# Kernel optimization log

Measured on AMD Instinct MI355X. Metric: run time of the kernel, lower is better.

## Reference

```python
import jax, jax.numpy as jnp
import numpy as np

D_HIDDEN = 1024
D_MODEL = 1024
R_MIN, R_MAX = 0.0, 1.0
MAX_PHASE = 6.28
SEQ_LEN = 16384


def setup_inputs() -> dict:
    key = jax.random.key(0)
    k_in, k_th, k_nu, k_bre, k_bim, k_cre, k_cim, k_d = jax.random.split(key, 8)
    inputs = jax.random.normal(k_in, (SEQ_LEN, D_MODEL), dtype=jnp.float32)
    # theta_log ~ log(max_phase * U)
    u_th = jax.random.uniform(k_th, (D_HIDDEN,), dtype=jnp.float32)
    theta_log = jnp.log(MAX_PHASE * u_th)
    # nu_log ~ log(-0.5 * log(U*(r_max^2 - r_min^2) + r_min^2))
    u_nu = jax.random.uniform(k_nu, (D_HIDDEN,), dtype=jnp.float32)
    nu_log = jnp.log(-0.5 * jnp.log(u_nu * (R_MAX**2 - R_MIN**2) + R_MIN**2))
    # gamma_log = log(sqrt(1 - |lambda|^2))
    diag_lambda = jnp.exp(-jnp.exp(nu_log) + 1j * jnp.exp(theta_log))
    gamma_log = jnp.log(jnp.sqrt(1.0 - jnp.abs(diag_lambda) ** 2))
    norm_b = jnp.sqrt(2.0 * D_MODEL)
    norm_c = jnp.sqrt(1.0 * D_HIDDEN)
    B_re = jax.random.normal(k_bre, (D_HIDDEN, D_MODEL), dtype=jnp.float32) / norm_b
    B_im = jax.random.normal(k_bim, (D_HIDDEN, D_MODEL), dtype=jnp.float32) / norm_b
    C_re = jax.random.normal(k_cre, (D_MODEL, D_HIDDEN), dtype=jnp.float32) / norm_c
    C_im = jax.random.normal(k_cim, (D_MODEL, D_HIDDEN), dtype=jnp.float32) / norm_c
    Dp = jax.random.normal(k_d, (D_MODEL,), dtype=jnp.float32)
    return {"inputs": inputs, "nu_log": nu_log, "theta_log": theta_log,
            "gamma_log": gamma_log, "B_re": B_re, "B_im": B_im,
            "C_re": C_re, "C_im": C_im, "Dp": Dp}


def _binop(q_i, q_j):
    # elementwise associative op for diagonal linear recurrence
    A_i, b_i = q_i
    A_j, b_j = q_j
    return (A_j * A_i, A_j * b_i + b_j)


def reference(inputs, nu_log, theta_log, gamma_log, B_re, B_im, C_re, C_im, Dp):
    # diag_lambda: [H] complex64
    diag_lambda = jnp.exp(-jnp.exp(nu_log) + 1j * jnp.exp(theta_log))
    B_norm = (B_re + 1j * B_im) * jnp.exp(gamma_log)[:, None]  # [H, D]
    C = C_re + 1j * C_im                                        # [D, H]
    L = inputs.shape[0]
    # Bu_t = B_norm @ x_t  -> [L, H] complex
    Bu = inputs.astype(B_norm.dtype) @ B_norm.T
    Lambda = jnp.broadcast_to(diag_lambda[None, :], (L, diag_lambda.shape[0]))
    # parallel scan of h_t = lambda * h_{t-1} + Bu_t (initial state = 0)
    _, hidden = jax.lax.associative_scan(_binop, (Lambda, Bu))  # [L, H]
    # y_t = Re[C h_t] + D * x_t
    outputs = jnp.real(hidden @ C.T) + Dp * inputs              # [L, D]
    return (hidden[-1:], outputs)
```

## Files before the change

kernel.cpp:

```cpp
#include <hip/hip_runtime.h>
#include <stdint.h>
#include <stddef.h>

typedef _Float16 f16;
typedef __attribute__((ext_vector_type(8))) _Float16 f16x8;
typedef __attribute__((ext_vector_type(4))) _Float16 f16x4;
typedef __attribute__((ext_vector_type(4))) float f32x4;
typedef __attribute__((ext_vector_type(2))) float f32x2;

#define L_SEQ 16384
#define DH    1024
#define DM    1024
#define NH2   2048
#define NC    256
#define LC    (L_SEQ / NC)

#define WSCALE     64.0f
#define INV_WSCALE 0.015625f

__device__ __forceinline__ void async_copy16(const void* g, void* l) {
  __builtin_amdgcn_global_load_lds((const __attribute__((address_space(1))) void*)g,
                                   (__attribute__((address_space(3))) void*)l,
                                   16, 0, 0);
}

__device__ __forceinline__ float h_lo(uint32_t w) {
  uint16_t u = (uint16_t)(w & 0xffffu); f16 h; __builtin_memcpy(&h, &u, 2); return (float)h;
}
__device__ __forceinline__ float h_hi(uint32_t w) {
  uint16_t u = (uint16_t)(w >> 16); f16 h; __builtin_memcpy(&h, &u, 2); return (float)h;
}

#define NB_CAST 8192
#define NB_W    1024
__global__ void k_prep_all(const float* __restrict__ x, f16* __restrict__ xb,
                           const float* __restrict__ B_re, const float* __restrict__ B_im,
                           const float* __restrict__ gamma_log, f16* __restrict__ Wcat,
                           const float* __restrict__ C_re, const float* __restrict__ C_im,
                           f16* __restrict__ Ccat,
                           const float* __restrict__ nu_log,
                           const float* __restrict__ theta_log,
                           float* __restrict__ lam_re, float* __restrict__ lam_im,
                           float* __restrict__ lamC_re, float* __restrict__ lamC_im) {
  const int b = blockIdx.x;
  if (b < NB_CAST) {
    int i = (b * 256 + (int)threadIdx.x) * 8;
    const float4 a0 = *(const float4*)(x + i);
    const float4 a1 = *(const float4*)(x + i + 4);
    f16x8 v;
    v[0] = (f16)a0.x; v[1] = (f16)a0.y; v[2] = (f16)a0.z; v[3] = (f16)a0.w;
    v[4] = (f16)a1.x; v[5] = (f16)a1.y; v[6] = (f16)a1.z; v[7] = (f16)a1.w;
    *(f16x8*)(xb + i) = v;
  } else if (b < NB_CAST + NB_W) {
    int idx = ((b - NB_CAST) * 256 + (int)threadIdx.x) * 4;
    int h = idx / DM;
    int d = idx - h * DM;
    float g = expf(gamma_log[h]) * WSCALE;
    float4 re = *(const float4*)(B_re + idx);
    float4 im = *(const float4*)(B_im + idx);
    f16x4 vr, vi;
    vr[0] = (f16)(re.x * g); vr[1] = (f16)(re.y * g);
    vr[2] = (f16)(re.z * g); vr[3] = (f16)(re.w * g);
    vi[0] = (f16)(im.x * g); vi[1] = (f16)(im.y * g);
    vi[2] = (f16)(im.z * g); vi[3] = (f16)(im.w * g);
    *(f16x4*)(Wcat + (size_t)(2 * h) * DM + d)     = vr;
    *(f16x4*)(Wcat + (size_t)(2 * h + 1) * DM + d) = vi;
  } else if (b < NB_CAST + 2 * NB_W) {
    int idx = ((b - NB_CAST - NB_W) * 256 + (int)threadIdx.x) * 4;
    int d = idx / DH;
    int k = idx - d * DH;
    float4 re = *(const float4*)(C_re + idx);
    float4 im = *(const float4*)(C_im + idx);
    f16x8 v;
    v[0] = (f16)re.x; v[1] = (f16)(-im.x);
    v[2] = (f16)re.y; v[3] = (f16)(-im.y);
    v[4] = (f16)re.z; v[5] = (f16)(-im.z);
    v[6] = (f16)re.w; v[7] = (f16)(-im.w);
    *(f16x8*)(Ccat + (size_t)d * NH2 + 2 * k) = v;
  } else {
    int h = (b - NB_CAST - 2 * NB_W) * 256 + (int)threadIdx.x;
    if (h < DH) {
      float nu  = expf(nu_log[h]);
      float th  = expf(theta_log[h]);
      float mag = expf(-nu);
      float lr = mag * cosf(th);
      float li = mag * sinf(th);
      lam_re[h] = lr; lam_im[h] = li;
      float ar = lr, ai = li;
#pragma unroll
      for (int i = 0; i < 6; ++i) {
        float nr = ar * ar - ai * ai;
        float ni = 2.f * ar * ai;
        ar = nr; ai = ni;
      }
      lamC_re[h] = ar; lamC_im[h] = ai;
    }
  }
}

template <int MODE>
__global__ __launch_bounds__(256, 3)
void k_gemm(const f16* __restrict__ A, const f16* __restrict__ B,
            void* __restrict__ Cout, const float* __restrict__ x,
            const float* __restrict__ dp,
            const float* __restrict__ lam_re, const float* __restrict__ lam_im,
            float* __restrict__ chunk_end, int K, int N) {
  __shared__ char smem[32768];
  f16* As = (f16*)smem;
  f16* Bs = (f16*)(smem + 16384);
  const int tid  = threadIdx.x;
  const int lane = tid & 63;
  const int wave = tid >> 6;
  const int wm = wave >> 1, wn = wave & 1;
  const int quad = lane >> 4;
  const int l16  = lane & 15;

  const int lin = blockIdx.y * gridDim.x + blockIdx.x;
  const int nY  = gridDim.y;
  const int per = 8 * nY;
  const int sg  = lin / per;
  const int r   = lin - sg * per;
  const int bx  = sg * 8 + (r & 7);
  const int by  = r >> 3;
  const int m0 = bx * 128;
  const int n0 = by * 128;

  f32x4 acc[4][4];
#pragma unroll
  for (int i = 0; i < 4; ++i)
#pragma unroll
    for (int j = 0; j < 4; ++j)
      acc[i][j] = f32x4{0.f, 0.f, 0.f, 0.f};

  for (int k0 = 0; k0 < K; k0 += 64) {
    __syncthreads();
#pragma unroll
    for (int q = 0; q < 4; ++q) {
      const int c = q * 256 + tid;
      const int row = c >> 3, slot = c & 7;
      const int part = slot ^ (row & 7);
      async_copy16(A + (size_t)(m0 + row) * K + k0 + part * 8, (char*)As + c * 16);
      async_copy16(B + (size_t)(n0 + row) * K + k0 + part * 8, (char*)Bs + c * 16);
    }
    __syncthreads();
#pragma unroll
    for (int kk = 0; kk < 64; kk += 32) {
      const int pbase = (kk >> 3);
      f16x8 fa[4], fb[4];
#pragma unroll
      for (int i = 0; i < 4; ++i) {
        const int ra = wm * 64 + i * 16 + l16;
        const int rb = wn * 64 + i * 16 + l16;
        const int sa = (pbase + quad) ^ (ra & 7);
        const int sb = (pbase + quad) ^ (rb & 7);
        fa[i] = *(const f16x8*)(As + ra * 64 + sa * 8);
        fb[i] = *(const f16x8*)(Bs + rb * 64 + sb * 8);
      }
#pragma unroll
      for (int i = 0; i < 4; ++i)
#pragma unroll
        for (int j = 0; j < 4; ++j)
          acc[i][j] = __builtin_amdgcn_mfma_f32_16x16x32_f16(fa[i], fb[j], acc[i][j], 0, 0, 0);
    }
  }

  if (MODE == 0) {
    __syncthreads();
    f16* T = (f16*)smem;
#pragma unroll
    for (int i = 0; i < 4; ++i)
#pragma unroll
      for (int j = 0; j < 4; ++j) {
        const int col = wn * 64 + j * 16 + l16;
        const int grp = col >> 3, cin = col & 7;
#pragma unroll
        for (int p = 0; p < 4; ++p) {
          const int row = wm * 64 + i * 16 + quad * 4 + p;
          T[row * 128 + ((grp ^ (row & 7)) << 3) + cin] = (f16)acc[i][j][p];
        }
      }
    __syncthreads();
    f16* out = (f16*)Cout;
    {
      const int row = tid >> 1, half = tid & 1;
#pragma unroll
      for (int o = 0; o < 8; ++o) {
        const int grp = half * 8 + o;
        f16x8 v = *(const f16x8*)(T + row * 128 + ((grp ^ (row & 7)) << 3));
        *(f16x8*)(out + (size_t)(m0 + row) * N + n0 + grp * 8) = v;
      }
    }
    if (tid < 128) {
      const int ck = tid >> 6;
      const int ch = tid & 63;
      const int gch = (n0 >> 1) + ch;
      const float lr = lam_re[gch], li = lam_im[gch];
      float hr = 0.f, hi = 0.f;
#pragma unroll 8
      for (int t = 0; t < 64; ++t) {
        const int row = ck * 64 + t;
        const int grpsw = ((ch >> 2) ^ (row & 7)) << 3;
        uint32_t w = *(const uint32_t*)(T + row * 128 + grpsw + ((2 * ch) & 7));
        float br = h_lo(w), bi = h_hi(w);
        float nr = lr * hr - li * hi + br;
        float ni = lr * hi + li * hr + bi;
        hr = nr; hi = ni;
      }
      *(f32x2*)(chunk_end + (size_t)(2 * bx + ck) * NH2 + n0 + 2 * ch) = f32x2{hr, hi};
    }
  } else {
    float* out = (float*)Cout;
    const int crow0 = m0 + wm * 64 + quad * 4;
    const int ccol0 = n0 + wn * 64 + l16;
#pragma unroll
    for (int j = 0; j < 4; ++j) {
      const int col = ccol0 + j * 16;
      const float dpv = dp[col];
#pragma unroll
      for (int i = 0; i < 4; ++i)
#pragma unroll
        for (int p = 0; p < 4; ++p) {
          const int row = crow0 + i * 16 + p;
          out[(size_t)row * N + col] = acc[i][j][p] + dpv * x[(size_t)row * N + col];
        }
    }
  }
}

__global__ void k_scan_carry(const float* __restrict__ chunk_end,
                             const float* __restrict__ lamC_re,
                             const float* __restrict__ lamC_im,
                             float* __restrict__ carry_in,
                             float* __restrict__ out_final,
                             int interleave) {
  const int h = blockIdx.x * 256 + threadIdx.x;
  const float lr = lamC_re[h], li = lamC_im[h];
  float er = 0.f, ei = 0.f;
#pragma unroll 16
  for (int c = 0; c < NC; ++c) {
    *(f32x2*)(carry_in + (size_t)c * NH2 + 2 * h) = f32x2{er, ei};
    f32x2 ce = *(const f32x2*)(chunk_end + (size_t)c * NH2 + 2 * h);
    float nr = lr * er - li * ei + ce[0];
    float ni = lr * ei + li * er + ce[1];
    er = nr; ei = ni;
  }
  if (interleave) {
    *(f32x2*)(out_final + 2 * h) = f32x2{er * INV_WSCALE, ei * INV_WSCALE};
  } else {
    out_final[h] = er * INV_WSCALE;
  }
}

__global__ void k_scan_apply(f16* __restrict__ Bu,
                             const float* __restrict__ lam_re,
                             const float* __restrict__ lam_im,
                             const float* __restrict__ carry_in) {
  const int colbase = (blockIdx.y * 256 + (int)threadIdx.x) * 4;
  const int c = blockIdx.x;
  const int h0 = colbase >> 1;
  const float lr0 = lam_re[h0],     li0 = lam_im[h0];
  const float lr1 = lam_re[h0 + 1], li1 = lam_im[h0 + 1];
  f32x4 cv = *(const f32x4*)(carry_in + (size_t)c * NH2 + colbase);
  float hr0 = cv[0], hi0 = cv[1], hr1 = cv[2], hi1 = cv[3];
  f16* p = Bu + (size_t)c * LC * NH2 + colbase;
#pragma unroll 4
  for (int t = 0; t < LC; ++t) {
    f16x4 b = *(const f16x4*)(p);
    float nr0 = lr0 * hr0 - li0 * hi0 + (float)b[0];
    float ni0 = lr0 * hi0 + li0 * hr0 + (float)b[1];
    float nr1 = lr1 * hr1 - li1 * hi1 + (float)b[2];
    float ni1 = lr1 * hi1 + li1 * hr1 + (float)b[3];
    hr0 = nr0; hi0 = ni0; hr1 = nr1; hi1 = ni1;
    f16x4 wv;
    wv[0] = (f16)(hr0 * INV_WSCALE); wv[1] = (f16)(hi0 * INV_WSCALE);
    wv[2] = (f16)(hr1 * INV_WSCALE); wv[3] = (f16)(hi1 * INV_WSCALE);
    *(f16x4*)(p) = wv;
    p += NH2;
  }
}


extern "C" void kernel_launch(void* const* d_in, const int* in_sizes, int n_in,
                              void* d_out, int out_size, void* d_ws, size_t ws_size,
                              hipStream_t stream) {
  const float* inputs    = (const float*)d_in[0];
  const float* nu_log    = (const float*)d_in[1];
  const float* theta_log = (const float*)d_in[2];
  const float* gamma_log = (const float*)d_in[3];
  const float* B_re      = (const float*)d_in[4];
  const float* B_im      = (const float*)d_in[5];
  const float* C_re      = (const float*)d_in[6];
  const float* C_im      = (const float*)d_in[7];
  const float* Dp        = (const float*)d_in[8];

  char* ws = (char*)d_ws;
  float* lam_re    = (float*)(ws + 0);
  float* lam_im    = (float*)(ws + 4096);
  float* lamC_re   = (float*)(ws + 8192);
  float* lamC_im   = (float*)(ws + 12288);
  float* chunk_end = (float*)(ws + 65536);
  float* carry_in  = (float*)(ws + 65536 + (2u << 20));
  f16*   Wcat      = (f16*)  (ws + 65536 + (4u << 20));
  f16*   Ccat      = (f16*)  (ws + 65536 + (8u << 20));
  f16*   Xb        = (f16*)  (ws + 65536 + (12u << 20));
  f16*   Bu        = (f16*)  (ws + 65536 + (44u << 20));

  int interleave = 1;
  int state_floats = 2048;
  if (out_size == 1024 + L_SEQ * DM) { interleave = 0; state_floats = 1024; }

  float* out_state = (float*)d_out;
  float* out_y     = (float*)d_out + state_floats;

  k_prep_all<<<dim3(NB_CAST + 2 * NB_W + 4), dim3(256), 0, stream>>>(
      inputs, Xb, B_re, B_im, gamma_log, Wcat, C_re, C_im, Ccat,
      nu_log, theta_log, lam_re, lam_im, lamC_re, lamC_im);

  k_gemm<0><<<dim3(L_SEQ / 128, NH2 / 128), dim3(256), 0, stream>>>(
      Xb, Wcat, (void*)Bu, nullptr, nullptr, lam_re, lam_im, chunk_end, DM, NH2);

  k_scan_carry<<<dim3(4), dim3(256), 0, stream>>>(chunk_end, lamC_re, lamC_im,
                                                  carry_in, out_state, interleave);
  k_scan_apply<<<dim3(NC, 2), dim3(256), 0, stream>>>(Bu, lam_re, lam_im, carry_in);

  k_gemm<1><<<dim3(L_SEQ / 128, DM / 128), dim3(256), 0, stream>>>(
      Bu, Ccat, (void*)out_y, inputs, Dp, nullptr, nullptr, nullptr, NH2, DM);

  (void)in_sizes; (void)n_in; (void)ws_size;
}
```

Measured before the change: 388.1 us.

## Use 256x256 GEMM tiles with 8 waves and double-buffered async LDS pipeline

Both GEMM instantiations move from 128x128 tiles with 4 waves to 256x256 tiles with 8 waves and 128KB of shared memory. The new K loop double-buffers LDS and issues global-to-LDS copies in quarter-tile steps interleaved with MFMA phases, coordinated by explicit vmcnt/lgkmcnt waits, barriers and setprio. The aim is to raise data reuse per tile and hide global load latency behind matrix math. In exchange, occupancy drops to one block per CU, and the grid for the second GEMM shrinks to 256 blocks, which can leave tail or load-imbalance effects. The epilogue and the per-chunk scan are rewritten for the larger tile.

```diff
diff --git a/kernel.cpp b/kernel.cpp
--- a/kernel.cpp
+++ b/kernel.cpp
@@ -99,21 +99,21 @@
 }
 
 template <int MODE>
-__global__ __launch_bounds__(256, 3)
+__global__ __launch_bounds__(512, 1)
 void k_gemm(const f16* __restrict__ A, const f16* __restrict__ B,
             void* __restrict__ Cout, const float* __restrict__ x,
             const float* __restrict__ dp,
             const float* __restrict__ lam_re, const float* __restrict__ lam_im,
             float* __restrict__ chunk_end, int K, int N) {
-  __shared__ char smem[32768];
-  f16* As = (f16*)smem;
-  f16* Bs = (f16*)(smem + 16384);
+  __shared__ char smem[131072];
   const int tid  = threadIdx.x;
   const int lane = tid & 63;
   const int wave = tid >> 6;
-  const int wm = wave >> 1, wn = wave & 1;
+  const int wm = wave >> 2;
+  const int wn = wave & 3;
   const int quad = lane >> 4;
   const int l16  = lane & 15;
+  const int k7   = l16 & 7;
 
   const int lin = blockIdx.y * gridDim.x + blockIdx.x;
   const int nY  = gridDim.y;
@@ -122,61 +122,152 @@
   const int r   = lin - sg * per;
   const int bx  = sg * 8 + (r & 7);
   const int by  = r >> 3;
-  const int m0 = bx * 128;
-  const int n0 = by * 128;
-
-  f32x4 acc[4][4];
-#pragma unroll
-  for (int i = 0; i < 4; ++i)
+  const int m0 = bx * 256;
+  const int n0 = by * 256;
+
+  const int NT = K >> 6;
+
+  f32x4 acc[8][4];
+#pragma unroll
+  for (int i = 0; i < 8; ++i)
 #pragma unroll
     for (int j = 0; j < 4; ++j)
       acc[i][j] = f32x4{0.f, 0.f, 0.f, 0.f};
 
-  for (int k0 = 0; k0 < K; k0 += 64) {
-    __syncthreads();
-#pragma unroll
-    for (int q = 0; q < 4; ++q) {
-      const int c = q * 256 + tid;
+  auto stage_half = [&](int H) {
+    if (H >= 4 * NT) return;
+    const int tau  = H >> 2;
+    const int part = H & 3;
+    const int d    = tau & 1;
+    const int kcol = tau << 6;
+    const f16* gsrc; int rbase; char* lbase;
+    if (part < 2) { gsrc = B; rbase = n0 + (part << 7);
+                    lbase = (char*)smem + d * 65536 + 32768 + (part << 14); }
+    else          { gsrc = A; rbase = m0 + ((part - 2) << 7);
+                    lbase = (char*)smem + d * 65536 + ((part - 2) << 14); }
+#pragma unroll
+    for (int q = 0; q < 2; ++q) {
+      const int c = (q << 9) + tid;
       const int row = c >> 3, slot = c & 7;
-      const int part = slot ^ (row & 7);
-      async_copy16(A + (size_t)(m0 + row) * K + k0 + part * 8, (char*)As + c * 16);
-      async_copy16(B + (size_t)(n0 + row) * K + k0 + part * 8, (char*)Bs + c * 16);
-    }
-    __syncthreads();
-#pragma unroll
-    for (int kk = 0; kk < 64; kk += 32) {
-      const int pbase = (kk >> 3);
-      f16x8 fa[4], fb[4];
-#pragma unroll
-      for (int i = 0; i < 4; ++i) {
-        const int ra = wm * 64 + i * 16 + l16;
-        const int rb = wn * 64 + i * 16 + l16;
-        const int sa = (pbase + quad) ^ (ra & 7);
-        const int sb = (pbase + quad) ^ (rb & 7);
-        fa[i] = *(const f16x8*)(As + ra * 64 + sa * 8);
-        fb[i] = *(const f16x8*)(Bs + rb * 64 + sb * 8);
-      }
-#pragma unroll
-      for (int i = 0; i < 4; ++i)
-#pragma unroll
-        for (int j = 0; j < 4; ++j)
-          acc[i][j] = __builtin_amdgcn_mfma_f32_16x16x32_f16(fa[i], fb[j], acc[i][j], 0, 0, 0);
-    }
+      const int p = slot ^ (row & 7);
+      async_copy16(gsrc + (size_t)(rbase + row) * K + kcol + (p << 3), lbase + c * 16);
+    }
+  };
+
+  for (int H = 0; H < 7; ++H) stage_half(H);
+  asm volatile("s_waitcnt vmcnt(6)" ::: "memory");
+  __builtin_amdgcn_s_barrier();
+
+  for (int t = 0; t < NT; ++t) {
+    const f16* Asd = (const f16*)((char*)smem + (t & 1) * 65536);
+    const f16* Bsd = Asd + 16384;
+
+    f16x8 bfr[4][2], afr[4][2];
+
+#pragma unroll
+    for (int nf = 0; nf < 4; ++nf) {
+      const int rb = (wn << 6) + (nf << 4) + l16;
+#pragma unroll
+      for (int kq = 0; kq < 2; ++kq) {
+        const int sb = ((kq << 2) | quad) ^ k7;
+        bfr[nf][kq] = *(const f16x8*)(Bsd + rb * 64 + sb * 8);
+      }
+    }
+#pragma unroll
+    for (int mf = 0; mf < 4; ++mf) {
+      const int ra = (wm << 7) + (mf << 4) + l16;
+#pragma unroll
+      for (int kq = 0; kq < 2; ++kq) {
+        const int sa = ((kq << 2) | quad) ^ k7;
+        afr[mf][kq] = *(const f16x8*)(Asd + ra * 64 + sa * 8);
+      }
+    }
+    stage_half(4 * t + 7);
+    __builtin_amdgcn_s_barrier();
+    asm volatile("s_waitcnt lgkmcnt(0)" ::: "memory");
+    __builtin_amdgcn_sched_barrier(0);
+    __builtin_amdgcn_s_setprio(1);
+#pragma unroll
+    for (int mf = 0; mf < 4; ++mf)
+#pragma unroll
+      for (int nf = 0; nf < 2; ++nf)
+#pragma unroll
+        for (int kq = 0; kq < 2; ++kq)
+          acc[mf][nf] = __builtin_amdgcn_mfma_f32_16x16x32_f16(afr[mf][kq], bfr[nf][kq], acc[mf][nf], 0, 0, 0);
+    __builtin_amdgcn_s_setprio(0);
+    __builtin_amdgcn_sched_barrier(0);
+    __builtin_amdgcn_s_barrier();
+
+    stage_half(4 * t + 8);
+    __builtin_amdgcn_s_barrier();
+    __builtin_amdgcn_s_setprio(1);
+#pragma unroll
+    for (int mf = 0; mf < 4; ++mf)
+#pragma unroll
+      for (int nf = 2; nf < 4; ++nf)
+#pragma unroll
+        for (int kq = 0; kq < 2; ++kq)
+          acc[mf][nf] = __builtin_amdgcn_mfma_f32_16x16x32_f16(afr[mf][kq], bfr[nf][kq], acc[mf][nf], 0, 0, 0);
+    __builtin_amdgcn_s_setprio(0);
+    __builtin_amdgcn_sched_barrier(0);
+    __builtin_amdgcn_s_barrier();
+
+#pragma unroll
+    for (int mf = 0; mf < 4; ++mf) {
+      const int ra = (wm << 7) + 64 + (mf << 4) + l16;
+#pragma unroll
+      for (int kq = 0; kq < 2; ++kq) {
+        const int sa = ((kq << 2) | quad) ^ k7;
+        afr[mf][kq] = *(const f16x8*)(Asd + ra * 64 + sa * 8);
+      }
+    }
+    stage_half(4 * t + 9);
+    __builtin_amdgcn_s_barrier();
+    asm volatile("s_waitcnt lgkmcnt(0)" ::: "memory");
+    __builtin_amdgcn_sched_barrier(0);
+    __builtin_amdgcn_s_setprio(1);
+#pragma unroll
+    for (int mf = 0; mf < 4; ++mf)
+#pragma unroll
+      for (int nf = 0; nf < 2; ++nf)
+#pragma unroll
+        for (int kq = 0; kq < 2; ++kq)
+          acc[4 + mf][nf] = __builtin_amdgcn_mfma_f32_16x16x32_f16(afr[mf][kq], bfr[nf][kq], acc[4 + mf][nf], 0, 0, 0);
+    __builtin_amdgcn_s_setprio(0);
+    __builtin_amdgcn_sched_barrier(0);
+    __builtin_amdgcn_s_barrier();
+
+    stage_half(4 * t + 10);
+    if (t == NT - 2) { asm volatile("s_waitcnt vmcnt(0)" ::: "memory"); }
+    else             { asm volatile("s_waitcnt vmcnt(6)" ::: "memory"); }
+    __builtin_amdgcn_s_barrier();
+    __builtin_amdgcn_s_setprio(1);
+#pragma unroll
+    for (int mf = 0; mf < 4; ++mf)
+#pragma unroll
+      for (int nf = 2; nf < 4; ++nf)
+#pragma unroll
+        for (int kq = 0; kq < 2; ++kq)
+          acc[4 + mf][nf] = __builtin_amdgcn_mfma_f32_16x16x32_f16(afr[mf][kq], bfr[nf][kq], acc[4 + mf][nf], 0, 0, 0);
+    __builtin_amdgcn_s_setprio(0);
+    __builtin_amdgcn_sched_barrier(0);
+    __builtin_amdgcn_s_barrier();
   }
 
   if (MODE == 0) {
+    asm volatile("s_waitcnt vmcnt(0)" ::: "memory");
     __syncthreads();
     f16* T = (f16*)smem;
 #pragma unroll
-    for (int i = 0; i < 4; ++i)
-#pragma unroll
-      for (int j = 0; j < 4; ++j) {
-        const int col = wn * 64 + j * 16 + l16;
+    for (int mf = 0; mf < 8; ++mf)
+#pragma unroll
+      for (int nf = 0; nf < 4; ++nf) {
+        const int col = (wn << 6) + (nf << 4) + l16;
         const int grp = col >> 3, cin = col & 7;
 #pragma unroll
         for (int p = 0; p < 4; ++p) {
-          const int row = wm * 64 + i * 16 + quad * 4 + p;
-          T[row * 128 + ((grp ^ (row & 7)) << 3) + cin] = (f16)acc[i][j][p];
+          const int row = (wm << 7) + (mf << 4) + (quad << 2) + p;
+          T[row * 256 + ((grp ^ (row & 7)) << 3) + cin] = (f16)acc[mf][nf][p];
         }
       }
     __syncthreads();
@@ -184,44 +275,44 @@
     {
       const int row = tid >> 1, half = tid & 1;
 #pragma unroll
-      for (int o = 0; o < 8; ++o) {
-        const int grp = half * 8 + o;
-        f16x8 v = *(const f16x8*)(T + row * 128 + ((grp ^ (row & 7)) << 3));
-        *(f16x8*)(out + (size_t)(m0 + row) * N + n0 + grp * 8) = v;
-      }
-    }
-    if (tid < 128) {
-      const int ck = tid >> 6;
-      const int ch = tid & 63;
+      for (int o = 0; o < 16; ++o) {
+        const int grp = (half << 4) + o;
+        f16x8 v = *(const f16x8*)(T + row * 256 + ((grp ^ (row & 7)) << 3));
+        *(f16x8*)(out + (size_t)(m0 + row) * N + n0 + (grp << 3)) = v;
+      }
+    }
+    {
+      const int ck = tid >> 7;
+      const int ch = tid & 127;
       const int gch = (n0 >> 1) + ch;
       const float lr = lam_re[gch], li = lam_im[gch];
       float hr = 0.f, hi = 0.f;
 #pragma unroll 8
-      for (int t = 0; t < 64; ++t) {
-        const int row = ck * 64 + t;
-        const int grpsw = ((ch >> 2) ^ (row & 7)) << 3;
-        uint32_t w = *(const uint32_t*)(T + row * 128 + grpsw + ((2 * ch) & 7));
+      for (int tt = 0; tt < 64; ++tt) {
+        const int row = (ck << 6) + tt;
+        const int sw = (((ch >> 2) ^ (row & 7)) << 3) + ((2 * ch) & 7);
+        uint32_t w = *(const uint32_t*)(T + row * 256 + sw);
         float br = h_lo(w), bi = h_hi(w);
         float nr = lr * hr - li * hi + br;
         float ni = lr * hi + li * hr + bi;
         hr = nr; hi = ni;
       }
-      *(f32x2*)(chunk_end + (size_t)(2 * bx + ck) * NH2 + n0 + 2 * ch) = f32x2{hr, hi};
+      *(f32x2*)(chunk_end + (size_t)((bx << 2) + ck) * NH2 + n0 + 2 * ch) = f32x2{hr, hi};
     }
   } else {
     float* out = (float*)Cout;
-    const int crow0 = m0 + wm * 64 + quad * 4;
-    const int ccol0 = n0 + wn * 64 + l16;
-#pragma unroll
-    for (int j = 0; j < 4; ++j) {
-      const int col = ccol0 + j * 16;
+    const int crow0 = m0 + (wm << 7) + (quad << 2);
+    const int ccol0 = n0 + (wn << 6) + l16;
+#pragma unroll
+    for (int nf = 0; nf < 4; ++nf) {
+      const int col = ccol0 + (nf << 4);
       const float dpv = dp[col];
 #pragma unroll
-      for (int i = 0; i < 4; ++i)
+      for (int mf = 0; mf < 8; ++mf)
 #pragma unroll
         for (int p = 0; p < 4; ++p) {
-          const int row = crow0 + i * 16 + p;
-          out[(size_t)row * N + col] = acc[i][j][p] + dpv * x[(size_t)row * N + col];
+          const int row = crow0 + (mf << 4) + p;
+          out[(size_t)row * N + col] = acc[mf][nf][p] + dpv * x[(size_t)row * N + col];
         }
     }
   }
@@ -316,14 +407,14 @@
       inputs, Xb, B_re, B_im, gamma_log, Wcat, C_re, C_im, Ccat,
       nu_log, theta_log, lam_re, lam_im, lamC_re, lamC_im);
 
-  k_gemm<0><<<dim3(L_SEQ / 128, NH2 / 128), dim3(256), 0, stream>>>(
+  k_gemm<0><<<dim3(L_SEQ / 256, NH2 / 256), dim3(512), 0, stream>>>(
       Xb, Wcat, (void*)Bu, nullptr, nullptr, lam_re, lam_im, chunk_end, DM, NH2);
 
   k_scan_carry<<<dim3(4), dim3(256), 0, stream>>>(chunk_end, lamC_re, lamC_im,
                                                   carry_in, out_state, interleave);
   k_scan_apply<<<dim3(NC, 2), dim3(256), 0, stream>>>(Bu, lam_re, lam_im, carry_in);
 
-  k_gemm<1><<<dim3(L_SEQ / 128, DM / 128), dim3(256), 0, stream>>>(
+  k_gemm<1><<<dim3(L_SEQ / 256, DM / 256), dim3(512), 0, stream>>>(
       Bu, Ccat, (void*)out_y, inputs, Dp, nullptr, nullptr, nullptr, NH2, DM);
 
   (void)in_sizes; (void)n_in; (void)ws_size;
```

After: 426.2 us. 1.1x slower.

## Parallelize chunk-carry scan with Hillis-Steele and read fp16 input in output epilogue

Applied to the files above, without the earlier changes.

The carry scan across chunks used to run on only 4 blocks, with each thread walking 256 chunks one after another. It now launches one block per hidden channel, with one thread per chunk, and runs a log-step Hillis-Steele scan in shared memory using powers of lambda^64. The output GEMM epilogue now reads the fp16 copy of the inputs instead of fp32 for the D*x skip term, which halves that read traffic. The fp16 skip term loses precision, and the log-depth scan changes the floating-point summation order.

```diff
diff --git a/kernel.cpp b/kernel.cpp
--- a/kernel.cpp
+++ b/kernel.cpp
@@ -101,7 +101,7 @@
 template <int MODE>
 __global__ __launch_bounds__(256, 3)
 void k_gemm(const f16* __restrict__ A, const f16* __restrict__ B,
-            void* __restrict__ Cout, const float* __restrict__ x,
+            void* __restrict__ Cout, const void* __restrict__ x,
             const float* __restrict__ dp,
             const float* __restrict__ lam_re, const float* __restrict__ lam_im,
             float* __restrict__ chunk_end, int K, int N) {
@@ -210,6 +210,7 @@
     }
   } else {
     float* out = (float*)Cout;
+    const f16* xb = (const f16*)x;
     const int crow0 = m0 + wm * 64 + quad * 4;
     const int ccol0 = n0 + wn * 64 + l16;
 #pragma unroll
@@ -221,7 +222,7 @@
 #pragma unroll
         for (int p = 0; p < 4; ++p) {
           const int row = crow0 + i * 16 + p;
-          out[(size_t)row * N + col] = acc[i][j][p] + dpv * x[(size_t)row * N + col];
+          out[(size_t)row * N + col] = acc[i][j][p] + dpv * (float)xb[(size_t)row * N + col];
         }
     }
   }
@@ -233,21 +234,37 @@
                              float* __restrict__ carry_in,
                              float* __restrict__ out_final,
                              int interleave) {
-  const int h = blockIdx.x * 256 + threadIdx.x;
-  const float lr = lamC_re[h], li = lamC_im[h];
-  float er = 0.f, ei = 0.f;
-#pragma unroll 16
-  for (int c = 0; c < NC; ++c) {
-    *(f32x2*)(carry_in + (size_t)c * NH2 + 2 * h) = f32x2{er, ei};
-    f32x2 ce = *(const f32x2*)(chunk_end + (size_t)c * NH2 + 2 * h);
-    float nr = lr * er - li * ei + ce[0];
-    float ni = lr * ei + li * er + ce[1];
-    er = nr; ei = ni;
-  }
-  if (interleave) {
-    *(f32x2*)(out_final + 2 * h) = f32x2{er * INV_WSCALE, ei * INV_WSCALE};
-  } else {
-    out_final[h] = er * INV_WSCALE;
+  __shared__ float sr[NC], si[NC];
+  const int h = blockIdx.x;
+  const int c = threadIdx.x;
+  f32x2 e = *(const f32x2*)(chunk_end + (size_t)c * NH2 + 2 * h);
+  float vr = e[0], vi = e[1];
+  float pr = lamC_re[h], pi = lamC_im[h];
+#pragma unroll
+  for (int s = 1; s < NC; s <<= 1) {
+    sr[c] = vr; si[c] = vi;
+    __syncthreads();
+    if (c >= s) {
+      const float ar = sr[c - s], ai = si[c - s];
+      vr += pr * ar - pi * ai;
+      vi += pr * ai + pi * ar;
+    }
+    __syncthreads();
+    const float nr = pr * pr - pi * pi;
+    const float ni = 2.f * pr * pi;
+    pr = nr; pi = ni;
+  }
+  sr[c] = vr; si[c] = vi;
+  __syncthreads();
+  const float er = (c == 0) ? 0.f : sr[c - 1];
+  const float ei = (c == 0) ? 0.f : si[c - 1];
+  *(f32x2*)(carry_in + (size_t)c * NH2 + 2 * h) = f32x2{er, ei};
+  if (c == NC - 1) {
+    if (interleave) {
+      *(f32x2*)(out_final + 2 * h) = f32x2{vr * INV_WSCALE, vi * INV_WSCALE};
+    } else {
+      out_final[h] = vr * INV_WSCALE;
+    }
   }
 }
 
@@ -319,12 +336,12 @@
   k_gemm<0><<<dim3(L_SEQ / 128, NH2 / 128), dim3(256), 0, stream>>>(
       Xb, Wcat, (void*)Bu, nullptr, nullptr, lam_re, lam_im, chunk_end, DM, NH2);
 
-  k_scan_carry<<<dim3(4), dim3(256), 0, stream>>>(chunk_end, lamC_re, lamC_im,
+  k_scan_carry<<<dim3(DH), dim3(NC), 0, stream>>>(chunk_end, lamC_re, lamC_im,
                                                   carry_in, out_state, interleave);
   k_scan_apply<<<dim3(NC, 2), dim3(256), 0, stream>>>(Bu, lam_re, lam_im, carry_in);
 
   k_gemm<1><<<dim3(L_SEQ / 128, DM / 128), dim3(256), 0, stream>>>(
-      Bu, Ccat, (void*)out_y, inputs, Dp, nullptr, nullptr, nullptr, NH2, DM);
+      Bu, Ccat, (void*)out_y, Xb, Dp, nullptr, nullptr, nullptr, NH2, DM);
 
   (void)in_sizes; (void)n_in; (void)ws_size;
 }
```

Result: faster. 343.5 us (-11.5%).
